# Kernel tuning notes

Measured on AMD Instinct MI355X. Metric: run time of the kernel, lower is better.

Reference implementation:

```python
import jax, jax.numpy as jnp
import numpy as np

N_WIRES = 4
DIM = 2 ** N_WIRES  # 16
# ZSIGN[w, b] = +1/-1 eigenvalue of Pauli-Z on wire w for basis state b (qubit 0 = MSB)
_bits = np.array([[(b >> (N_WIRES - 1 - w)) & 1 for b in range(DIM)] for w in range(N_WIRES)])
ZSIGN = jnp.asarray(1.0 - 2.0 * _bits, dtype=jnp.float32)  # [4, 16]
CNOT4 = jnp.asarray(np.array([[1, 0, 0, 0], [0, 1, 0, 0], [0, 0, 0, 1], [0, 0, 1, 0]], dtype=np.float32))


def _apply_1q(state, U2, w):
    # state [..., 16]; apply 2x2 gate U2 on wire w
    batch = state.shape[:-1]
    s = state.reshape(batch + (2,) * N_WIRES)
    s = jnp.moveaxis(s, w - N_WIRES, -1)
    s = s @ U2.astype(s.dtype).T
    s = jnp.moveaxis(s, -1, w - N_WIRES)
    return s.reshape(batch + (DIM,))


def _apply_2q(state, U4, c, t):
    # state [..., 16]; apply 4x4 gate U4 on wires (c=control-axis-first, t)
    batch = state.shape[:-1]
    s = state.reshape(batch + (2,) * N_WIRES)
    s = jnp.moveaxis(s, (c - N_WIRES, t - N_WIRES), (-2, -1))
    sh = s.shape
    s = s.reshape(sh[:-2] + (4,))
    s = s @ U4.astype(s.dtype).T
    s = s.reshape(sh)
    s = jnp.moveaxis(s, (-2, -1), (c - N_WIRES, t - N_WIRES))
    return s.reshape(batch + (DIM,))


def _product_state(qs):
    # kron of per-qubit 2-vectors -> [..., 16]
    s = qs[0]
    for q in qs[1:]:
        o = s[..., :, None] * q[..., None, :]
        s = o.reshape(o.shape[:-2] + (o.shape[-2] * o.shape[-1],))
    return s


def _measure_z(state):
    if jnp.iscomplexobj(state):
        probs = state.real ** 2 + state.imag ** 2
    else:
        probs = state ** 2
    return probs.astype(jnp.float32) @ ZSIGN.T  # [..., 4]


def _quanv(x, rl_params):
    # x [B, 784]; 2x2 stride-2 patches of 28x28 image, RY encode, fixed 8-op
    # 'random layer' (RY(rl_params[w]) on wire w then CNOT(w, w+1 mod 4)), measure Z.
    B = x.shape[0]
    img = x.reshape(B, 14, 2, 14, 2)
    patches = img.transpose(0, 1, 3, 2, 4).reshape(B, 196, 4)  # [(r,c),(r,c+1),(r+1,c),(r+1,c+1)]
    half = patches * 0.5
    q = jnp.stack([jnp.cos(half), jnp.sin(half)], axis=-1)  # RY(theta)|0> is real, [B,196,4,2]
    st = _product_state([q[..., w, :] for w in range(N_WIRES)])  # [B,196,16] float32
    for w in range(N_WIRES):
        th = rl_params[w] * 0.5
        ct, sn = jnp.cos(th), jnp.sin(th)
        U2 = jnp.stack([jnp.stack([ct, -sn]), jnp.stack([sn, ct])])
        st = _apply_1q(st, U2, w)
        st = _apply_2q(st, CNOT4, w, (w + 1) % N_WIRES)
    return _measure_z(st)  # [B, 196, 4]


def _qlayer(ang, theta):
    # RX(ang_w) encode + trainable RX(theta_w) fuse into RX(ang+theta); CNOT ring; <Z>
    half = (ang + theta) * 0.5  # [B, 4]
    c = jnp.cos(half).astype(jnp.complex64)
    s = (-1j) * jnp.sin(half).astype(jnp.complex64)
    q = jnp.stack([c, s], axis=-1)  # [B, 4, 2]
    st = _product_state([q[:, w, :] for w in range(N_WIRES)])  # [B, 16] complex64
    for w in range(N_WIRES):
        st = _apply_2q(st, CNOT4, w, (w + 1) % N_WIRES)
    return _measure_z(st)  # [B, 4]


def _forward(x, rl_params, lin_W, lin_b, qtheta):
    B = x.shape[0]
    qfeat = _quanv(x, rl_params)  # [B, 196, 4]
    xs = jnp.transpose(qfeat, (1, 0, 2))  # [196, B, 4] sequence for quantum LSTM
    h0 = jnp.zeros((B, 4), jnp.float32)
    c0 = jnp.zeros((B, 4), jnp.float32)

    def step(carry, xt):
        hx, cx = carry
        comb = jnp.concatenate([xt, hx], axis=1)  # [B, 8]
        f = jax.nn.sigmoid(_qlayer(comb @ lin_W[0] + lin_b[0], qtheta[0]))
        i = jax.nn.sigmoid(_qlayer(comb @ lin_W[1] + lin_b[1], qtheta[1]))
        g = jnp.tanh(_qlayer(comb @ lin_W[2] + lin_b[2], qtheta[2]))
        o = jax.nn.sigmoid(_qlayer(comb @ lin_W[3] + lin_b[3], qtheta[3]))
        cx = f * cx + i * g
        hx = o * jnp.tanh(cx)
        return (hx, cx), hx

    (hx, cx), _ = jax.lax.scan(step, (h0, c0), xs)
    # torch.tensor([float(v) ...]) detaches -> stop_gradient; mean over batch
    w = jax.lax.stop_gradient(jnp.mean(hx, axis=0))  # [4]
    # EstimatorQNN: ry(inp_i) then rx(w_i) per qubit, observable ZZZZ -> prod cos(inp)cos(w)
    inp = x[:, :N_WIRES]
    return jnp.prod(jnp.cos(inp) * jnp.cos(w), axis=1, keepdims=True)  # [B, 1]


def setup_inputs() -> dict:
    key = jax.random.key(0)
    k0, k1, k2, k3 = jax.random.split(key, 4)
    B = 8192
    x = jax.random.uniform(k0, (B, 784), dtype=jnp.float32) * np.float32(np.pi)
    rl_params = jax.random.normal(k1, (4,), dtype=jnp.float32)
    lin_W = jax.random.normal(k2, (4, 8, 4), dtype=jnp.float32) * np.float32(1.0 / np.sqrt(8.0))
    lin_b = jnp.zeros((4, 4), dtype=jnp.float32)
    qtheta = jax.random.normal(k3, (4, 4), dtype=jnp.float32)
    return {"x": x, "rl_params": rl_params, "lin_W": lin_W, "lin_b": lin_b, "qtheta": qtheta}


def reference(x, rl_params, lin_W, lin_b, qtheta):
    return _forward(x, rl_params, lin_W, lin_b, qtheta)
```

## Files before the change

### kernel.cpp

```cpp
#include <hip/hip_runtime.h>
#include <math.h>

#define NPATCH 196
#define QROWS  200

typedef unsigned short ushort_t;

__device__ __forceinline__ float fast_rcp(float x) { return __builtin_amdgcn_rcpf(x); }
__device__ __forceinline__ float sigm(float x)      { return fast_rcp(1.0f + __expf(-x)); }
__device__ __forceinline__ float tanh_fast(float x) { return fmaf(-2.0f, fast_rcp(1.0f + __expf(2.0f * x)), 1.0f); }

__device__ __forceinline__ ushort_t f2bf(float f) {
    unsigned u = __float_as_uint(f);
    u += 0x7FFFu + ((u >> 16) & 1u);
    return (ushort_t)(u >> 16);
}
__device__ __forceinline__ float bf2f(ushort_t h) { return __uint_as_float((unsigned)h << 16); }

template<int CTRL>
__device__ __forceinline__ float qperm(float x) {
    int i = __float_as_int(x);
    int r = __builtin_amdgcn_update_dpp(i, i, CTRL, 0xF, 0xF, true);
    return __int_as_float(r);
}
#define QP_BCAST0 0x00
#define QP_BCAST1 0x55
#define QP_BCAST2 0xAA
#define QP_BCAST3 0xFF
#define QP_XOR1   0xB1
#define QP_XOR2   0x4E

#define SPB  16
#define ROWP 788

__global__ __launch_bounds__(256) void quanv_kernel(const float* __restrict__ x,
                                                    const float* __restrict__ rl,
                                                    ushort_t* __restrict__ qfeat, int B)
{
    __shared__ float tile[SPB][ROWP];
    const int tid = threadIdx.x;
    const int b0  = blockIdx.x * SPB;

#pragma unroll 4
    for (int r = 0; r < SPB; ++r) {
        if (tid < 196) {
            ((float4*)&tile[r][0])[tid] =
                ((const float4*)(x + (size_t)(b0 + r) * 784))[tid];
        }
    }
    __syncthreads();

    float rs[4], rc[4];
#pragma unroll
    for (int w = 0; w < 4; ++w) __sincosf(rl[w] * 0.5f, &rs[w], &rc[w]);

    const int s  = tid & 15;
    const int tg = tid >> 4;
    const float* row = &tile[s][0];

    for (int t = tg; t < NPATCH; t += 16) {
        int i = t / 14, j = t - i * 14;
        int o = i * 56 + j * 2;
        float a[4] = { row[o], row[o + 1], row[o + 28], row[o + 29] };

        float cw[4], sw[4];
#pragma unroll
        for (int w = 0; w < 4; ++w) __sincosf(a[w] * 0.5f, &sw[w], &cw[w]);

        float amp[16];
#pragma unroll
        for (int idx = 0; idx < 16; ++idx) {
            float v = ((idx & 8) ? sw[0] : cw[0]) * ((idx & 4) ? sw[1] : cw[1]);
            v *= ((idx & 2) ? sw[2] : cw[2]);
            v *= ((idx & 1) ? sw[3] : cw[3]);
            amp[idx] = v;
        }

#pragma unroll
        for (int w = 0; w < 4; ++w) {
            const int mask = 8 >> w;
#pragma unroll
            for (int idx = 0; idx < 16; ++idx) {
                if (!(idx & mask)) {
                    float a0 = amp[idx], a1 = amp[idx | mask];
                    amp[idx]        = rc[w] * a0 - rs[w] * a1;
                    amp[idx | mask] = rs[w] * a0 + rc[w] * a1;
                }
            }
            const int tmask = 8 >> ((w + 1) & 3);
#pragma unroll
            for (int idx = 0; idx < 16; ++idx) {
                if ((idx & mask) && !(idx & tmask)) {
                    float tmp = amp[idx];
                    amp[idx] = amp[idx | tmask];
                    amp[idx | tmask] = tmp;
                }
            }
        }

        float p[16];
#pragma unroll
        for (int idx = 0; idx < 16; ++idx) p[idx] = amp[idx] * amp[idx];
        float z0 = 0.f, z1 = 0.f, z2 = 0.f, z3 = 0.f;
#pragma unroll
        for (int idx = 0; idx < 16; ++idx) {
            z0 += (idx & 8) ? -p[idx] : p[idx];
            z1 += (idx & 4) ? -p[idx] : p[idx];
            z2 += (idx & 2) ? -p[idx] : p[idx];
            z3 += (idx & 1) ? -p[idx] : p[idx];
        }

        ushort4 outv;
        outv.x = f2bf(z0); outv.y = f2bf(z1); outv.z = f2bf(z2); outv.w = f2bf(z3);
        *(ushort4*)(qfeat + ((size_t)t * B + (b0 + s)) * 4) = outv;
    }
}

__global__ __launch_bounds__(64) void lstm_kernel(const ushort_t* __restrict__ qfeat,
                                                  const float* __restrict__ lin_W,
                                                  const float* __restrict__ lin_b,
                                                  const float* __restrict__ qtheta,
                                                  float* __restrict__ sums, int B)
{
    int gid = blockIdx.x * 64 + threadIdx.x;
    int smp = gid >> 2;
    int u   = gid & 3;

    float W[4][8], bt[4];
#pragma unroll
    for (int k = 0; k < 4; ++k) {
#pragma unroll
        for (int j = 0; j < 8; ++j) W[k][j] = lin_W[(k * 8 + j) * 4 + u];
        bt[k] = lin_b[k * 4 + u] + qtheta[k * 4 + u];
    }

    const ushort4* qf = (const ushort4*)qfeat;
    ushort4 r0 = qf[(size_t)0 * B + smp];
    ushort4 r1 = qf[(size_t)1 * B + smp];
    ushort4 r2 = qf[(size_t)2 * B + smp];
    ushort4 r3 = qf[(size_t)3 * B + smp];

    float cx = 0.f, hx = 0.f;

    auto step = [&](ushort4& buf, int tn) {
        float xt0 = bf2f(buf.x), xt1 = bf2f(buf.y), xt2 = bf2f(buf.z), xt3 = bf2f(buf.w);
        buf = qf[(size_t)tn * B + smp];

        float h0 = qperm<QP_BCAST0>(hx);
        float h1 = qperm<QP_BCAST1>(hx);
        float h2 = qperm<QP_BCAST2>(hx);
        float h3 = qperm<QP_BCAST3>(hx);

        float z[4];
#pragma unroll
        for (int k = 0; k < 4; ++k) {
            float s0 = fmaf(xt0, W[k][0], bt[k]);
            float s1 = xt1 * W[k][1];
            s0 = fmaf(xt2, W[k][2], s0);
            s1 = fmaf(xt3, W[k][3], s1);
            s0 = fmaf(h0, W[k][4], s0);
            s1 = fmaf(h1, W[k][5], s1);
            s0 = fmaf(h2, W[k][6], s0);
            s1 = fmaf(h3, W[k][7], s1);
            float cv = __cosf(s0 + s1);
            float sx1 = qperm<QP_XOR1>(cv);
            float m1  = cv * sx1;
            float sx2 = qperm<QP_XOR2>(m1);
            float zz = (u == 0) ? sx1 * sx2
                     : (u == 1) ? m1
                     : (u == 2) ? cv * sx2
                                : m1 * sx2;
            z[k] = zz;
        }
        float f  = sigm(z[0]);
        float ii = sigm(z[1]);
        float g  = tanh_fast(z[2]);
        float o  = sigm(z[3]);
        cx = fmaf(f, cx, ii * g);
        hx = o * tanh_fast(cx);
    };

    for (int t = 0; t < NPATCH; t += 4) {
        step(r0, t + 4);
        step(r1, t + 5);
        step(r2, t + 6);
        step(r3, t + 7);
    }

    float v = hx;
#pragma unroll
    for (int m = 4; m < 64; m <<= 1) v += __shfl_xor(v, m, 64);
    if ((threadIdx.x & 63) < 4) atomicAdd(sums + u, v);
}

__global__ __launch_bounds__(256) void final_kernel(const float* __restrict__ x,
                                                    const float* __restrict__ sums,
                                                    float* __restrict__ out,
                                                    int B, float invB)
{
    int b = blockIdx.x * blockDim.x + threadIdx.x;
    if (b >= B) return;
    float P = cosf(sums[0] * invB) * cosf(sums[1] * invB) *
              cosf(sums[2] * invB) * cosf(sums[3] * invB);
    const float4 xi = *(const float4*)(x + (size_t)b * 784);
    out[b] = P * cosf(xi.x) * cosf(xi.y) * cosf(xi.z) * cosf(xi.w);
}

extern "C" void kernel_launch(void* const* d_in, const int* in_sizes, int n_in,
                              void* d_out, int out_size, void* d_ws, size_t ws_size,
                              hipStream_t stream)
{
    const float* x      = (const float*)d_in[0];
    const float* rl     = (const float*)d_in[1];
    const float* lin_W  = (const float*)d_in[2];
    const float* lin_b  = (const float*)d_in[3];
    const float* qtheta = (const float*)d_in[4];
    float* out = (float*)d_out;
    int B = in_sizes[0] / 784;

    float*    sums  = (float*)d_ws;
    ushort_t* qfeat = (ushort_t*)((char*)d_ws + 256);

    hipMemsetAsync(sums, 0, 4 * sizeof(float), stream);

    quanv_kernel<<<B / SPB, 256, 0, stream>>>(x, rl, qfeat, B);

    lstm_kernel<<<(B * 4) / 64, 64, 0, stream>>>(qfeat, lin_W, lin_b, qtheta, sums, B);

    final_kernel<<<(B + 255) / 256, 256, 0, stream>>>(x, sums, out, B, 1.0f / (float)B);
}
```

Measured before the change: 176.2 us.

## Spread LSTM gates across 16 lanes per sample using row-rotate DPP

The LSTM kernel now gives each sample 16 lanes (4 hidden units x 4 gates) instead of 4. Each lane computes one gate pre-activation, forms the Z-product from row-rotated cosines, and applies a unified sigmoid/tanh, and the gates are then broadcast with DPP. This shortens the serial per-step dependency chain and raises parallelism for the 196-step recurrence. The prefetch depth grows from 4 to 7 steps. The trade-off is 4x more threads, redundant cell-state work across lanes, and more DPP traffic. Because 196 = 7x28, the loop prefetches up to index 202, past the 196 written rows, and QROWS is bumped to 204 to cover those reads.

```diff
diff --git a/kernel.cpp b/kernel.cpp
--- a/kernel.cpp
+++ b/kernel.cpp
@@ -2,7 +2,7 @@
 #include <math.h>
 
 #define NPATCH 196
-#define QROWS  200
+#define QROWS  204
 
 typedef unsigned short ushort_t;
 
@@ -18,17 +18,20 @@
 __device__ __forceinline__ float bf2f(ushort_t h) { return __uint_as_float((unsigned)h << 16); }
 
 template<int CTRL>
-__device__ __forceinline__ float qperm(float x) {
-    int i = __float_as_int(x);
-    int r = __builtin_amdgcn_update_dpp(i, i, CTRL, 0xF, 0xF, true);
-    return __int_as_float(r);
+__device__ __forceinline__ int dpp_i(int x) {
+    return __builtin_amdgcn_update_dpp(x, x, CTRL, 0xF, 0xF, true);
+}
+template<int CTRL>
+__device__ __forceinline__ float dpp_f(float x) {
+    return __int_as_float(dpp_i<CTRL>(__float_as_int(x)));
 }
 #define QP_BCAST0 0x00
 #define QP_BCAST1 0x55
 #define QP_BCAST2 0xAA
 #define QP_BCAST3 0xFF
-#define QP_XOR1   0xB1
-#define QP_XOR2   0x4E
+#define ROR4      0x124
+#define ROR8      0x128
+#define ROR12     0x12C
 
 #define SPB  16
 #define ROWP 788
@@ -116,29 +119,52 @@
     }
 }
 
-__global__ __launch_bounds__(64) void lstm_kernel(const ushort_t* __restrict__ qfeat,
-                                                  const float* __restrict__ lin_W,
-                                                  const float* __restrict__ lin_b,
-                                                  const float* __restrict__ qtheta,
-                                                  float* __restrict__ sums, int B)
-{
-    int gid = blockIdx.x * 64 + threadIdx.x;
-    int smp = gid >> 2;
-    int u   = gid & 3;
-
-    float W[4][8], bt[4];
-#pragma unroll
-    for (int k = 0; k < 4; ++k) {
-#pragma unroll
-        for (int j = 0; j < 8; ++j) W[k][j] = lin_W[(k * 8 + j) * 4 + u];
-        bt[k] = lin_b[k * 4 + u] + qtheta[k * 4 + u];
-    }
+__global__ __launch_bounds__(256) void lstm_kernel(const ushort_t* __restrict__ qfeat,
+                                                   const float* __restrict__ lin_W,
+                                                   const float* __restrict__ lin_b,
+                                                   const float* __restrict__ qtheta,
+                                                   float* __restrict__ sums, int B)
+{
+    const int tid = threadIdx.x;
+    const int gid = blockIdx.x * 256 + tid;
+    const int smp = gid >> 4;
+    const int u   = (tid >> 2) & 3;
+    const int k   = tid & 3;
+
+    const int j1 = dpp_i<ROR4>(u);
+    const int j2 = dpp_i<ROR8>(u);
+    const int j3 = dpp_i<ROR12>(u);
+
+    float Wx0 = lin_W[(k * 8 + 0) * 4 + u];
+    float Wx1 = lin_W[(k * 8 + 1) * 4 + u];
+    float Wx2 = lin_W[(k * 8 + 2) * 4 + u];
+    float Wx3 = lin_W[(k * 8 + 3) * 4 + u];
+    float Wh0 = lin_W[(k * 8 + 4 + u)  * 4 + u];
+    float Wh1 = lin_W[(k * 8 + 4 + j1) * 4 + u];
+    float Wh2 = lin_W[(k * 8 + 4 + j2) * 4 + u];
+    float Wh3 = lin_W[(k * 8 + 4 + j3) * 4 + u];
+    float bt  = lin_b[k * 4 + u] + qtheta[k * 4 + u];
+
+    auto in_set = [](int j, int uu) {
+        return (uu == 0) ? (j != 0) : (uu == 1) ? (j <= 1) : (uu == 2) ? (j <= 2) : true;
+    };
+    const bool inc0 = in_set(u,  u);
+    const bool inc1 = in_set(j1, u);
+    const bool inc2 = in_set(j2, u);
+    const bool inc3 = in_set(j3, u);
+
+    const float mlt = (k == 2) ?  2.0f : -1.0f;
+    const float ga  = (k == 2) ? -2.0f :  1.0f;
+    const float gb  = (k == 2) ?  1.0f :  0.0f;
 
     const ushort4* qf = (const ushort4*)qfeat;
     ushort4 r0 = qf[(size_t)0 * B + smp];
     ushort4 r1 = qf[(size_t)1 * B + smp];
     ushort4 r2 = qf[(size_t)2 * B + smp];
     ushort4 r3 = qf[(size_t)3 * B + smp];
+    ushort4 r4 = qf[(size_t)4 * B + smp];
+    ushort4 r5 = qf[(size_t)5 * B + smp];
+    ushort4 r6 = qf[(size_t)6 * B + smp];
 
     float cx = 0.f, hx = 0.f;
 
@@ -146,51 +172,55 @@
         float xt0 = bf2f(buf.x), xt1 = bf2f(buf.y), xt2 = bf2f(buf.z), xt3 = bf2f(buf.w);
         buf = qf[(size_t)tn * B + smp];
 
-        float h0 = qperm<QP_BCAST0>(hx);
-        float h1 = qperm<QP_BCAST1>(hx);
-        float h2 = qperm<QP_BCAST2>(hx);
-        float h3 = qperm<QP_BCAST3>(hx);
-
-        float z[4];
-#pragma unroll
-        for (int k = 0; k < 4; ++k) {
-            float s0 = fmaf(xt0, W[k][0], bt[k]);
-            float s1 = xt1 * W[k][1];
-            s0 = fmaf(xt2, W[k][2], s0);
-            s1 = fmaf(xt3, W[k][3], s1);
-            s0 = fmaf(h0, W[k][4], s0);
-            s1 = fmaf(h1, W[k][5], s1);
-            s0 = fmaf(h2, W[k][6], s0);
-            s1 = fmaf(h3, W[k][7], s1);
-            float cv = __cosf(s0 + s1);
-            float sx1 = qperm<QP_XOR1>(cv);
-            float m1  = cv * sx1;
-            float sx2 = qperm<QP_XOR2>(m1);
-            float zz = (u == 0) ? sx1 * sx2
-                     : (u == 1) ? m1
-                     : (u == 2) ? cv * sx2
-                                : m1 * sx2;
-            z[k] = zz;
-        }
-        float f  = sigm(z[0]);
-        float ii = sigm(z[1]);
-        float g  = tanh_fast(z[2]);
-        float o  = sigm(z[3]);
-        cx = fmaf(f, cx, ii * g);
+        float hr1 = dpp_f<ROR4>(hx);
+        float hr2 = dpp_f<ROR8>(hx);
+        float hr3 = dpp_f<ROR12>(hx);
+
+        float s0 = fmaf(xt0, Wx0, bt);
+        float s1 = xt1 * Wx1;
+        s0 = fmaf(xt2, Wx2, s0);
+        s1 = fmaf(xt3, Wx3, s1);
+        s0 = fmaf(hx,  Wh0, s0);
+        s1 = fmaf(hr1, Wh1, s1);
+        s0 = fmaf(hr2, Wh2, s0);
+        s1 = fmaf(hr3, Wh3, s1);
+        float cv = __cosf(s0 + s1);
+
+        float c1 = dpp_f<ROR4>(cv);
+        float c2 = dpp_f<ROR8>(cv);
+        float c3 = dpp_f<ROR12>(cv);
+        float t0 = inc0 ? cv : 1.0f;
+        float t1 = inc1 ? c1 : 1.0f;
+        float t2 = inc2 ? c2 : 1.0f;
+        float t3 = inc3 ? c3 : 1.0f;
+        float z  = (t0 * t1) * (t2 * t3);
+
+        float e  = __expf(z * mlt);
+        float gv = fmaf(fast_rcp(1.0f + e), ga, gb);
+
+        float f  = dpp_f<QP_BCAST0>(gv);
+        float ii = dpp_f<QP_BCAST1>(gv);
+        float gg = dpp_f<QP_BCAST2>(gv);
+        float o  = dpp_f<QP_BCAST3>(gv);
+
+        cx = fmaf(f, cx, ii * gg);
         hx = o * tanh_fast(cx);
     };
 
-    for (int t = 0; t < NPATCH; t += 4) {
-        step(r0, t + 4);
-        step(r1, t + 5);
-        step(r2, t + 6);
-        step(r3, t + 7);
+    for (int t = 0; t < NPATCH; t += 7) {
+        step(r0, t + 7);
+        step(r1, t + 8);
+        step(r2, t + 9);
+        step(r3, t + 10);
+        step(r4, t + 11);
+        step(r5, t + 12);
+        step(r6, t + 13);
     }
 
     float v = hx;
-#pragma unroll
-    for (int m = 4; m < 64; m <<= 1) v += __shfl_xor(v, m, 64);
-    if ((threadIdx.x & 63) < 4) atomicAdd(sums + u, v);
+    v += __shfl_xor(v, 16, 64);
+    v += __shfl_xor(v, 32, 64);
+    if ((tid & 63) < 16 && k == 0) atomicAdd(sums + u, v);
 }
 
 __global__ __launch_bounds__(256) void final_kernel(const float* __restrict__ x,
@@ -225,7 +255,7 @@
 
     quanv_kernel<<<B / SPB, 256, 0, stream>>>(x, rl, qfeat, B);
 
-    lstm_kernel<<<(B * 4) / 64, 64, 0, stream>>>(qfeat, lin_W, lin_b, qtheta, sums, B);
+    lstm_kernel<<<(B * 16) / 256, 256, 0, stream>>>(qfeat, lin_W, lin_b, qtheta, sums, B);
 
     final_kernel<<<(B + 255) / 256, 256, 0, stream>>>(x, sums, out, B, 1.0f / (float)B);
 }
```

After: 148.0 us. -16.0%, faster.
